# Performance work log

Hardware: AMD Instinct MI355X
Metric: run time of the kernel (lower is better)

Reference implementation:

```python
import jax, jax.numpy as jnp
import numpy as np
from jax import lax

S, V, DW = 2048, 50000, 400     # seq_len, word vocab, word emb dim
CV, DC = 8, 32                  # casing vocab / dim
PV, DP = 50, 64                 # POS vocab / dim
H, C = 768, 13                  # lstm hidden (per direction), num tag classes
DIN = DW + DC + DP              # 496 lstm input dim


def setup_inputs() -> dict:
    key = jax.random.key(0)
    ks = jax.random.split(key, 18)
    r = lambda k, sh, s=0.02: (jax.random.normal(k, sh) * s).astype(jnp.float32)
    return {
        "x": jax.random.randint(ks[0], (S,), 0, V),
        "casing": jax.random.randint(ks[1], (S,), 0, CV),
        "pos": jax.random.randint(ks[2], (S,), 0, PV),
        "word_emb": r(ks[3], (V, DW)),
        "casing_emb": r(ks[4], (CV, DC)),
        "pos_emb": r(ks[5], (PV, DP)),
        "Wih_f": r(ks[6], (4 * H, DIN)),
        "Whh_f": r(ks[7], (4 * H, H)),
        "b_f": jnp.zeros((4 * H,), jnp.float32),
        "Wih_b": r(ks[8], (4 * H, DIN)),
        "Whh_b": r(ks[9], (4 * H, H)),
        "b_b": jnp.zeros((4 * H,), jnp.float32),
        "Wc": r(ks[10], (C, 2 * H)),
        "bc": jnp.zeros((C,), jnp.float32),
        "start_trans": r(ks[11], (C,), 0.1),
        "end_trans": r(ks[12], (C,), 0.1),
        "trans": r(ks[13], (C, C), 0.1),
        "h0": jnp.zeros((2, H), jnp.float32),
        "c0": jnp.zeros((2, H), jnp.float32),
    }


def _lstm(xg, Whh, h0, c0):
    # xg: (S, 4H) precomputed input-to-hidden gates; PyTorch gate order i,f,g,o
    def step(carry, g_in):
        h, c = carry
        g = g_in + h @ Whh.T
        i, f, gg, o = jnp.split(g, 4)
        c = jax.nn.sigmoid(f) * c + jax.nn.sigmoid(i) * jnp.tanh(gg)
        h = jax.nn.sigmoid(o) * jnp.tanh(c)
        return (h, c), h
    _, hs = lax.scan(step, (h0, c0), xg)
    return hs  # (S, H)


def reference(x, casing, pos, word_emb, casing_emb, pos_emb,
              Wih_f, Whh_f, b_f, Wih_b, Whh_b, b_b, Wc, bc,
              start_trans, end_trans, trans, h0, c0):
    # embedding concat -> (S, DIN)
    emb = jnp.concatenate([word_emb[x], casing_emb[casing], pos_emb[pos]], axis=-1)
    # weight-dropped LSTM (eval mode: DropConnect identity), bidirectional
    hs_f = _lstm(emb @ Wih_f.T + b_f, Whh_f, h0[0], c0[0])
    hs_b = _lstm((emb @ Wih_b.T + b_b)[::-1], Whh_b, h0[1], c0[1])[::-1]
    o = jnp.concatenate([hs_f, hs_b], axis=-1) @ Wc.T + bc  # (S, C)
    tag_scores = jax.nn.log_softmax(o, axis=1)
    # CRF Viterbi decode (torchcrf-style), batch of 1 (the unsqueeze(0))
    score0 = start_trans + tag_scores[0]
    def vstep(score, em):
        cand = score[:, None] + trans            # (prev C, next C)
        bp = jnp.argmax(cand, axis=0)
        return jnp.max(cand, axis=0) + em, bp
    score, bps = lax.scan(vstep, score0, tag_scores[1:])
    last = jnp.argmax(score + end_trans)
    def back(tag, bp):
        prev = bp[tag]
        return prev, prev
    _, prevs = lax.scan(back, last, bps[::-1])
    tags = jnp.concatenate([prevs[::-1], last[None]])  # (S,) best path
    return tag_scores, tags
```

## Files before the change

kernel.cpp:

```cpp
#include <hip/hip_runtime.h>
#include <hip/hip_bf16.h>


#define SEQ  2048
#define DINW 496
#define HDIM 768
#define G4   3072
#define CDIM 13
#define NWG  48
#define JPW  16
#define DATA_SPIN (1u << 14)
#define LDK  40

typedef __attribute__((ext_vector_type(8))) short bf16x8;
typedef __attribute__((ext_vector_type(4))) float f32x4;

__device__ __forceinline__ float sigf(float x) { return 1.0f / (1.0f + __expf(-x)); }
__device__ __forceinline__ float tanhf_fast(float x) {
    float ax = fabsf(x);
    float e  = __expf(-2.0f * ax);
    float t  = (1.0f - e) / (1.0f + e);
    return copysignf(t, x);
}
__device__ __forceinline__ unsigned pack_bf16(float a, float b) {
    union { __hip_bfloat16 h; unsigned short u; } x, y;
    x.h = __float2bfloat16(a); y.h = __float2bfloat16(b);
    return (unsigned)x.u | ((unsigned)y.u << 16);
}

__global__ __launch_bounds__(256) void k_gemm_xg(
    const int* __restrict__ x, const int* __restrict__ casing, const int* __restrict__ pos,
    const float* __restrict__ we, const float* __restrict__ ce, const float* __restrict__ pe,
    const float* __restrict__ Wih_f, const float* __restrict__ b_f,
    const float* __restrict__ Wih_b, const float* __restrict__ b_b,
    __hip_bfloat16* __restrict__ xg_f, __hip_bfloat16* __restrict__ xg_b)
{
    __shared__ unsigned short Ab[128][LDK];
    __shared__ unsigned short Bb[128][LDK];
    int dir = blockIdx.z;
    const float* B    = dir ? Wih_b : Wih_f;
    const float* bias = dir ? b_b   : b_f;
    __hip_bfloat16* C = dir ? xg_b  : xg_f;
    int n0 = blockIdx.x * 128, m0 = blockIdx.y * 128;
    int tid = threadIdx.x;
    int r = tid & 127, half = tid >> 7;
    int lane = tid & 63, wv = tid >> 6;
    int wr = wv >> 1, wc = wv & 1;
    int lrow = lane & 15, kg = lane >> 4;

    int m = m0 + r;
    const float* arow_w = we + (size_t)x[m] * 400;
    const float* arow_c = ce + (size_t)casing[m] * 32;
    const float* arow_p = pe + (size_t)pos[m] * 64;
    const float* brow   = B + (size_t)(n0 + r) * DINW;

    f32x4 acc[4][4] = {};

    for (int it = 0; it < 16; it++) {
        int kb = it * 32 + half * 16;
        float av[16], bv[16];
        if (kb >= DINW) {
            #pragma unroll
            for (int i = 0; i < 16; i++) { av[i] = 0.f; bv[i] = 0.f; }
        } else {
            #pragma unroll
            for (int c4 = 0; c4 < 4; c4++) {
                int k = kb + c4 * 4;
                float4 v;
                if (k < 400)      v = *(const float4*)(arow_w + k);
                else if (k < 432) v = *(const float4*)(arow_c + (k - 400));
                else              v = *(const float4*)(arow_p + (k - 432));
                av[c4 * 4 + 0] = v.x; av[c4 * 4 + 1] = v.y;
                av[c4 * 4 + 2] = v.z; av[c4 * 4 + 3] = v.w;
                float4 u = *(const float4*)(brow + k);
                bv[c4 * 4 + 0] = u.x; bv[c4 * 4 + 1] = u.y;
                bv[c4 * 4 + 2] = u.z; bv[c4 * 4 + 3] = u.w;
            }
        }
        unsigned pa[8], pb[8];
        #pragma unroll
        for (int i = 0; i < 8; i++) {
            pa[i] = pack_bf16(av[2 * i], av[2 * i + 1]);
            pb[i] = pack_bf16(bv[2 * i], bv[2 * i + 1]);
        }
        __syncthreads();
        uint4* dA = (uint4*)&Ab[r][half * 16];
        uint4* dB = (uint4*)&Bb[r][half * 16];
        dA[0] = make_uint4(pa[0], pa[1], pa[2], pa[3]);
        dA[1] = make_uint4(pa[4], pa[5], pa[6], pa[7]);
        dB[0] = make_uint4(pb[0], pb[1], pb[2], pb[3]);
        dB[1] = make_uint4(pb[4], pb[5], pb[6], pb[7]);
        __syncthreads();

        union frag { uint4 u; bf16x8 v; };
        frag af[4], bf[4];
        #pragma unroll
        for (int i = 0; i < 4; i++) {
            int arow = wr * 64 + i * 16 + lrow;
            int bcol = wc * 64 + i * 16 + lrow;
            af[i].u = *(const uint4*)((const char*)&Ab[0][0] + arow * (LDK * 2) + kg * 16);
            bf[i].u = *(const uint4*)((const char*)&Bb[0][0] + bcol * (LDK * 2) + kg * 16);
        }
        #pragma unroll
        for (int i = 0; i < 4; i++)
            #pragma unroll
            for (int j = 0; j < 4; j++)
                acc[i][j] = __builtin_amdgcn_mfma_f32_16x16x32_bf16(
                                af[i].v, bf[j].v, acc[i][j], 0, 0, 0);
    }

    #pragma unroll
    for (int j = 0; j < 4; j++) {
        int col = n0 + wc * 64 + j * 16 + lrow;
        float bsv = bias[col];
        #pragma unroll
        for (int i = 0; i < 4; i++) {
            int rbase = m0 + wr * 64 + i * 16 + kg * 4;
            #pragma unroll
            for (int reg = 0; reg < 4; reg++)
                C[(size_t)(rbase + reg) * G4 + col] =
                    __float2bfloat16(acc[i][j][reg] + bsv);
        }
    }
}

__global__ __launch_bounds__(1024) void k_lstm(
    const __hip_bfloat16* __restrict__ xg_f, const __hip_bfloat16* __restrict__ xg_b,
    const float* __restrict__ Whh_f, const float* __restrict__ Whh_b,
    const float* __restrict__ h0, const float* __restrict__ c0v,
    float* __restrict__ hs_f, float* __restrict__ hs_b,
    unsigned* __restrict__ msg, unsigned* __restrict__ abortw)
{
    __shared__ float hbuf[2][HDIM];
    __shared__ unsigned sbuf[16];
    __shared__ unsigned sdead;

    int wg = blockIdx.x;
    int dir = wg & 1, slot = wg >> 1;
    const __hip_bfloat16* xg = dir ? xg_b : xg_f;
    const float* Whh = dir ? Whh_b : Whh_f;
    float* hs        = dir ? hs_b  : hs_f;
    unsigned* mdir = msg + (size_t)dir * 2 * HDIM;

    int tid = threadIdx.x, lane = tid & 63, wv = tid >> 6;
    int q = lane >> 4, gl = lane & 15;
    int j = slot * JPW + wv;

    float w[48];
    const float* wr = Whh + (size_t)(q * HDIM + j) * HDIM;
    #pragma unroll
    for (int m = 0; m < 12; m++) {
        float4 f4 = *(const float4*)(wr + gl * 4 + m * 64);
        w[m * 4 + 0] = f4.x; w[m * 4 + 1] = f4.y;
        w[m * 4 + 2] = f4.z; w[m * 4 + 3] = f4.w;
    }
    float cst = c0v[dir * HDIM + j];

    if (tid == 0) sdead = 0;

    for (int t = 0; t < SEQ; t++) {
        int xrow = dir ? (SEQ - 1 - t) : t;
        const __hip_bfloat16* xga = xg + (size_t)xrow * G4 + j;
        float xv0 = __bfloat162float(xga[0]);
        float xv1 = __bfloat162float(xga[HDIM]);
        float xv2 = __bfloat162float(xga[2 * HDIM]);
        float xv3 = __bfloat162float(xga[3 * HDIM]);

        int par = (t & 1) ^ 1;

        if (wv < 2) {
            int base = wv * 6;
            if (t == 0) {
                #pragma unroll
                for (int m = 0; m < 6; m++)
                    hbuf[1][(base + m) * 64 + lane] = h0[dir * HDIM + (base + m) * 64 + lane];
            } else {
                const unsigned* g = mdir + (size_t)par * HDIM;
                unsigned vals[6];
                unsigned fresh = 0, rounds = 0;
                bool dead = false;
                for (;;) {
                    #pragma unroll
                    for (int m = 0; m < 6; m++)
                        if (!(fresh & (1u << m)))
                            vals[m] = __hip_atomic_load(&g[(base + m) * 64 + lane],
                                        __ATOMIC_RELAXED, __HIP_MEMORY_SCOPE_AGENT);
                    #pragma unroll
                    for (int m = 0; m < 6; m++)
                        if ((vals[m] >> 16) == (unsigned)t) fresh |= (1u << m);
                    if (__all(fresh == 0x3Fu)) break;
                    unsigned ab = __hip_atomic_load(abortw,
                                    __ATOMIC_RELAXED, __HIP_MEMORY_SCOPE_AGENT);
                    if (ab || ++rounds >= DATA_SPIN) { dead = true; break; }
                }
                #pragma unroll
                for (int m = 0; m < 6; m++) {
                    union { unsigned u; float f; } cvt;
                    cvt.u = (vals[m] & 0xFFFFu) << 16;
                    hbuf[par][(base + m) * 64 + lane] = cvt.f;
                }
                if (dead && lane == 0) {
                    __hip_atomic_store(abortw, 1u,
                                       __ATOMIC_RELAXED, __HIP_MEMORY_SCOPE_AGENT);
                    sdead = 1;
                }
            }
        }

        __syncthreads();
        if (sdead) break;

        float acc = 0.f;
        #pragma unroll
        for (int m = 0; m < 12; m++) {
            float4 f4 = *(const float4*)&hbuf[par][gl * 4 + m * 64];
            acc += w[m * 4 + 0] * f4.x + w[m * 4 + 1] * f4.y
                 + w[m * 4 + 2] * f4.z + w[m * 4 + 3] * f4.w;
        }
        acc += __shfl_xor(acc, 1);
        acc += __shfl_xor(acc, 2);
        acc += __shfl_xor(acc, 4);
        acc += __shfl_xor(acc, 8);
        float si = __shfl(acc, 0),  sf = __shfl(acc, 16);
        float sg = __shfl(acc, 32), so = __shfl(acc, 48);

        float gi = sigf(xv0 + si), gf = sigf(xv1 + sf);
        float gg = tanhf_fast(xv2 + sg), go = sigf(xv3 + so);
        cst = gf * cst + gi * gg;
        float h = go * tanhf_fast(cst);

        if (lane == 0) {
            union { __hip_bfloat16 b; unsigned short u; } cv;
            cv.b = __float2bfloat16(h);
            sbuf[wv] = ((unsigned)(t + 1) << 16) | (unsigned)cv.u;
            int hrow = dir ? (SEQ - 1 - t) : t;
            hs[(size_t)hrow * HDIM + j] = h;
        }
        __syncthreads();

        if (wv == 0 && lane < 16)
            __hip_atomic_store(&mdir[(size_t)(t & 1) * HDIM + slot * JPW + lane],
                               sbuf[lane],
                               __ATOMIC_RELAXED, __HIP_MEMORY_SCOPE_AGENT);
    }
}

__global__ __launch_bounds__(256) void k_head(
    const float* __restrict__ hs_f, const float* __restrict__ hs_b,
    const float* __restrict__ Wc, const float* __restrict__ bc,
    float* __restrict__ out)
{
    __shared__ float wcs[CDIM][1536];
    __shared__ float bcs[CDIM];
    int tid = threadIdx.x;
    for (int i = tid; i < CDIM * 1536; i += 256) {
        int n = i / 1536;
        wcs[n][i - n * 1536] = Wc[i];
    }
    if (tid < CDIM) bcs[tid] = bc[tid];
    __syncthreads();

    int lane = tid & 63, wv = tid >> 6;
    int off = (lane < 32) ? lane * 24 : 768 + (lane - 32) * 24;
    for (int rr = 0; rr < 4; rr++) {
        int row = blockIdx.x * 16 + wv * 4 + rr;
        const float* src = (lane < 32) ? (hs_f + (size_t)row * HDIM + lane * 24)
                                       : (hs_b + (size_t)row * HDIM + (lane - 32) * 24);
        float hvv[24];
        #pragma unroll
        for (int k = 0; k < 6; k++) {
            float4 f4 = *(const float4*)(src + k * 4);
            hvv[k * 4 + 0] = f4.x; hvv[k * 4 + 1] = f4.y;
            hvv[k * 4 + 2] = f4.z; hvv[k * 4 + 3] = f4.w;
        }
        float o[CDIM];
        #pragma unroll
        for (int n = 0; n < CDIM; n++) {
            const float* wr2 = &wcs[n][off];
            float s0 = 0.f, s1 = 0.f, s2 = 0.f, s3 = 0.f;
            #pragma unroll
            for (int k = 0; k < 6; k++) {
                float4 w4 = *(const float4*)(wr2 + k * 4);
                s0 += w4.x * hvv[k * 4 + 0];
                s1 += w4.y * hvv[k * 4 + 1];
                s2 += w4.z * hvv[k * 4 + 2];
                s3 += w4.w * hvv[k * 4 + 3];
            }
            o[n] = (s0 + s1) + (s2 + s3);
        }
        #pragma unroll
        for (int n = 0; n < CDIM; n++) {
            #pragma unroll
            for (int d = 1; d < 64; d <<= 1) o[n] += __shfl_xor(o[n], d);
            o[n] += bcs[n];
        }
        float m = o[0];
        #pragma unroll
        for (int n = 1; n < CDIM; n++) m = fmaxf(m, o[n]);
        float sum = 0.f;
        #pragma unroll
        for (int n = 0; n < CDIM; n++) sum += __expf(o[n] - m);
        float ls = m + __logf(sum);
        if (lane == 0) {
            #pragma unroll
            for (int n = 0; n < CDIM; n++) out[(size_t)row * CDIM + n] = o[n] - ls;
        }
    }
}

__global__ __launch_bounds__(64) void k_viterbi(
    const float* __restrict__ ts, const float* __restrict__ st,
    const float* __restrict__ en, const float* __restrict__ tr,
    float* __restrict__ tags_out)
{
    __shared__ unsigned char bp[SEQ - 1][16];
    __shared__ unsigned char path[SEQ];
    int n = threadIdx.x;
    bool act = n < CDIM;
    float trn[CDIM];
    #pragma unroll
    for (int p = 0; p < CDIM; p++) trn[p] = act ? tr[p * CDIM + n] : -1e30f;
    float score = act ? (st[n] + ts[n]) : -1e30f;

    for (int s = 1; s < SEQ; s++) {
        float em = act ? ts[(size_t)s * CDIM + n] : 0.f;
        float sp[CDIM];
        #pragma unroll
        for (int p = 0; p < CDIM; p++) sp[p] = __shfl(score, p);
        float best = -1e30f; int arg = 0;
        #pragma unroll
        for (int p = 0; p < CDIM; p++) {
            float v = sp[p] + trn[p];
            if (v > best) { best = v; arg = p; }
        }
        score = best + em;
        if (act) bp[s - 1][n] = (unsigned char)arg;
    }
    float fin = act ? (score + en[n]) : -1e30f;
    float fv[CDIM];
    #pragma unroll
    for (int p = 0; p < CDIM; p++) fv[p] = __shfl(fin, p);
    __syncthreads();
    if (n == 0) {
        float best = -1e30f; int last = 0;
        #pragma unroll
        for (int p = 0; p < CDIM; p++) { if (fv[p] > best) { best = fv[p]; last = p; } }
        int cur = last;
        path[SEQ - 1] = (unsigned char)cur;
        for (int s = SEQ - 2; s >= 0; s--) { cur = bp[s][cur]; path[s] = (unsigned char)cur; }
    }
    __syncthreads();
    for (int i = n; i < SEQ; i += 64) tags_out[i] = (float)path[i];
}

__global__ void k_zero(float* p, int n) {
    int i = blockIdx.x * 256 + threadIdx.x;
    if (i < n) p[i] = 0.f;
}

extern "C" void kernel_launch(void* const* d_in, const int* in_sizes, int n_in,
                              void* d_out, int out_size, void* d_ws, size_t ws_size,
                              hipStream_t stream)
{
    const int*   x      = (const int*)d_in[0];
    const int*   casing = (const int*)d_in[1];
    const int*   pos    = (const int*)d_in[2];
    const float* we     = (const float*)d_in[3];
    const float* ce     = (const float*)d_in[4];
    const float* pe     = (const float*)d_in[5];
    const float* Wih_f  = (const float*)d_in[6];
    const float* Whh_f  = (const float*)d_in[7];
    const float* b_f    = (const float*)d_in[8];
    const float* Wih_b  = (const float*)d_in[9];
    const float* Whh_b  = (const float*)d_in[10];
    const float* b_b    = (const float*)d_in[11];
    const float* Wc     = (const float*)d_in[12];
    const float* bc     = (const float*)d_in[13];
    const float* strt   = (const float*)d_in[14];
    const float* endt   = (const float*)d_in[15];
    const float* trans  = (const float*)d_in[16];
    const float* h0     = (const float*)d_in[17];
    const float* c0     = (const float*)d_in[18];

    const size_t need = 37761028;
    if (ws_size < need) {
        k_zero<<<(out_size + 255) / 256, 256, 0, stream>>>((float*)d_out, out_size);
        return;
    }
    char* wsb = (char*)d_ws;
    float* hs_f = (float*)(wsb);
    float* hs_b = (float*)(wsb + 6291456);
    __hip_bfloat16* xg_f = (__hip_bfloat16*)(wsb + 12582912);
    __hip_bfloat16* xg_b = (__hip_bfloat16*)(wsb + 25165824);
    unsigned* msg = (unsigned*)(wsb + 37748736);
    unsigned* abortw = (unsigned*)(wsb + 37761024);

    hipMemsetAsync(msg, 0, 12288 + 4, stream);

    k_gemm_xg<<<dim3(G4 / 128, SEQ / 128, 2), 256, 0, stream>>>(
        x, casing, pos, we, ce, pe, Wih_f, b_f, Wih_b, b_b, xg_f, xg_b);
    k_lstm<<<2 * NWG, 1024, 0, stream>>>(
        xg_f, xg_b, Whh_f, Whh_b, h0, c0, hs_f, hs_b, msg, abortw);
    k_head<<<SEQ / 16, 256, 0, stream>>>(hs_f, hs_b, Wc, bc, (float*)d_out);
    k_viterbi<<<1, 64, 0, stream>>>(
        (const float*)d_out, strt, endt, trans, (float*)d_out + (size_t)SEQ * CDIM);
}
```

Measured before the change: 5.990 ms.

## Pin each LSTM direction's workgroups to a single XCC via dynamic slot claiming

The LSTM kernel now launches many more workgroups than it needs. Each workgroup reads its hardware XCC ID and atomically claims a slot, so that all forward-direction workgroups land on XCC 0 and all backward ones on XCC 1. Workgroups that get no slot exit early, with a fallback that takes leftover slots from other XCCs. The aim is to keep each direction's per-step cross-workgroup h exchange inside one XCC's L2, which cuts the cost of cross-die coherence in the sequential recurrence. In exchange it adds launch overhead for many idle blocks and relies on hardware scheduling and co-residency.

```diff
diff --git a/kernel.cpp b/kernel.cpp
--- a/kernel.cpp
+++ b/kernel.cpp
@@ -129,20 +129,63 @@
     const float* __restrict__ Whh_f, const float* __restrict__ Whh_b,
     const float* __restrict__ h0, const float* __restrict__ c0v,
     float* __restrict__ hs_f, float* __restrict__ hs_b,
-    unsigned* __restrict__ msg, unsigned* __restrict__ abortw)
+    unsigned* __restrict__ msg, unsigned* __restrict__ abortw,
+    unsigned* __restrict__ claim)
 {
     __shared__ float hbuf[2][HDIM];
     __shared__ unsigned sbuf[16];
     __shared__ unsigned sdead;
-
-    int wg = blockIdx.x;
-    int dir = wg & 1, slot = wg >> 1;
+    __shared__ unsigned sslot;
+
+    int tid = threadIdx.x, lane = tid & 63, wv = tid >> 6;
+
+    unsigned xcc;
+    asm("s_getreg_b32 %0, hwreg(HW_REG_XCC_ID)" : "=s"(xcc));
+    xcc &= 7u;
+    if (tid == 0) {
+        unsigned enc = 0;
+        if (xcc < 2u) {
+            unsigned idx = atomicAdd(&claim[xcc], 1u);
+            if (idx < (unsigned)NWG) enc = (xcc << 16) | (idx + 1u);
+        }
+        if (enc == 0) {
+            for (int it = 0; it < 1024; ++it) {
+                unsigned c0 = __hip_atomic_load(&claim[0], __ATOMIC_RELAXED,
+                                                __HIP_MEMORY_SCOPE_AGENT);
+                unsigned c1 = __hip_atomic_load(&claim[1], __ATOMIC_RELAXED,
+                                                __HIP_MEMORY_SCOPE_AGENT);
+                if (c0 >= (unsigned)NWG && c1 >= (unsigned)NWG) break;
+                __builtin_amdgcn_s_sleep(16);
+            }
+            unsigned c0 = __hip_atomic_load(&claim[0], __ATOMIC_RELAXED,
+                                            __HIP_MEMORY_SCOPE_AGENT);
+            if (c0 < (unsigned)NWG) {
+                unsigned idx = atomicAdd(&claim[0], 1u);
+                if (idx < (unsigned)NWG) enc = (0u << 16) | (idx + 1u);
+            }
+            if (enc == 0) {
+                unsigned c1 = __hip_atomic_load(&claim[1], __ATOMIC_RELAXED,
+                                                __HIP_MEMORY_SCOPE_AGENT);
+                if (c1 < (unsigned)NWG) {
+                    unsigned idx = atomicAdd(&claim[1], 1u);
+                    if (idx < (unsigned)NWG) enc = (1u << 16) | (idx + 1u);
+                }
+            }
+        }
+        sslot = enc;
+        sdead = 0;
+    }
+    __syncthreads();
+    unsigned enc = sslot;
+    if (enc == 0) return;
+    int dir  = (int)(enc >> 16);
+    int slot = (int)(enc & 0xFFFFu) - 1;
+
     const __hip_bfloat16* xg = dir ? xg_b : xg_f;
     const float* Whh = dir ? Whh_b : Whh_f;
     float* hs        = dir ? hs_b  : hs_f;
     unsigned* mdir = msg + (size_t)dir * 2 * HDIM;
 
-    int tid = threadIdx.x, lane = tid & 63, wv = tid >> 6;
     int q = lane >> 4, gl = lane & 15;
     int j = slot * JPW + wv;
 
@@ -155,8 +198,6 @@
         w[m * 4 + 2] = f4.z; w[m * 4 + 3] = f4.w;
     }
     float cst = c0v[dir * HDIM + j];
-
-    if (tid == 0) sdead = 0;
 
     for (int t = 0; t < SEQ; t++) {
         int xrow = dir ? (SEQ - 1 - t) : t;
@@ -382,7 +423,7 @@
     const float* h0     = (const float*)d_in[17];
     const float* c0     = (const float*)d_in[18];
 
-    const size_t need = 37761028;
+    const size_t need = 37761060;
     if (ws_size < need) {
         k_zero<<<(out_size + 255) / 256, 256, 0, stream>>>((float*)d_out, out_size);
         return;
@@ -392,15 +433,16 @@
     float* hs_b = (float*)(wsb + 6291456);
     __hip_bfloat16* xg_f = (__hip_bfloat16*)(wsb + 12582912);
     __hip_bfloat16* xg_b = (__hip_bfloat16*)(wsb + 25165824);
-    unsigned* msg = (unsigned*)(wsb + 37748736);
+    unsigned* msg    = (unsigned*)(wsb + 37748736);
     unsigned* abortw = (unsigned*)(wsb + 37761024);
-
-    hipMemsetAsync(msg, 0, 12288 + 4, stream);
+    unsigned* claim  = (unsigned*)(wsb + 37761028);
+
+    hipMemsetAsync(msg, 0, 12288 + 4 + 32, stream);
 
     k_gemm_xg<<<dim3(G4 / 128, SEQ / 128, 2), 256, 0, stream>>>(
         x, casing, pos, we, ce, pe, Wih_f, b_f, Wih_b, b_b, xg_f, xg_b);
-    k_lstm<<<2 * NWG, 1024, 0, stream>>>(
-        xg_f, xg_b, Whh_f, Whh_b, h0, c0, hs_f, hs_b, msg, abortw);
+    k_lstm<<<2048, 1024, 0, stream>>>(
+        xg_f, xg_b, Whh_f, Whh_b, h0, c0, hs_f, hs_b, msg, abortw, claim);
     k_head<<<SEQ / 16, 256, 0, stream>>>(hs_f, hs_b, Wc, bc, (float*)d_out);
     k_viterbi<<<1, 64, 0, stream>>>(
         (const float*)d_out, strt, endt, trans, (float*)d_out + (size_t)SEQ * CDIM);
```

Result: slower. 6.580 ms (+9.9%).
